# Performance work log

Measured on AMD Instinct MI355X. Metric: run time of the kernel, lower is better.

Reference implementation:

```python
import jax, jax.numpy as jnp
import numpy as np

D_K = 1024
NHEADS = 16
HEAD_DIM = D_K // NHEADS  # 64
STD = float(np.sqrt(HEAD_DIM))  # matches math.sqrt(d_k // nheads)


def setup_inputs() -> dict:
    key = jax.random.key(0)
    ks = jax.random.split(key, 9)
    B, S = 2, 2048
    scale = 1.0 / np.sqrt(D_K)
    x = jax.random.normal(ks[0], (B, S, D_K), dtype=jnp.float32)
    Wq = jax.random.normal(ks[1], (D_K, D_K), dtype=jnp.float32) * scale
    bq = jnp.zeros((D_K,), dtype=jnp.float32)
    Wk = jax.random.normal(ks[2], (D_K, D_K), dtype=jnp.float32) * scale
    bk = jnp.zeros((D_K,), dtype=jnp.float32)
    Wv = jax.random.normal(ks[3], (D_K, D_K), dtype=jnp.float32) * scale
    bv = jnp.zeros((D_K,), dtype=jnp.float32)
    Wo = jax.random.normal(ks[4], (D_K, D_K), dtype=jnp.float32) * scale
    bo = jnp.zeros((D_K,), dtype=jnp.float32)
    return {"x": x, "Wq": Wq, "bq": bq, "Wk": Wk, "bk": bk,
            "Wv": Wv, "bv": bv, "Wo": Wo, "bo": bo}


def _heads(x, W, b):
    # Linear then split heads: (B,S,D) -> (B,H,S,hd)
    B, S, _ = x.shape
    out = x @ W.T + b
    return out.reshape(B, S, NHEADS, HEAD_DIM).transpose(0, 2, 1, 3)


def reference(x, Wq, bq, Wk, bk, Wv, bv, Wo, bo):
    B, S, _ = x.shape
    q = _heads(x, Wq, bq)  # (B,H,S,hd)
    k = _heads(x, Wk, bk)
    v = _heads(x, Wv, bv)
    scores = jnp.einsum('bhqd,bhkd->bhqk', q, k) / STD  # (B,H,S,S)
    causal = jnp.tril(jnp.ones((S, S), dtype=bool))  # mask_factory default
    scores = jnp.where(causal[None, None, :, :], scores, -jnp.inf)
    attn = jax.nn.softmax(scores, axis=-1)
    ctx = jnp.einsum('bhqk,bhkd->bhqd', attn, v)  # (B,H,S,hd)
    ctx = ctx.transpose(0, 2, 1, 3).reshape(B, S, D_K)
    return ctx @ Wo.T + bo
```

## Files before the change

kernel.cpp:

```cpp
#include <hip/hip_runtime.h>
#include <stdint.h>

typedef unsigned short u16;
typedef __bf16 bf16x8 __attribute__((ext_vector_type(8)));
typedef __bf16 bf16x4v __attribute__((ext_vector_type(4)));
typedef float f32x4 __attribute__((ext_vector_type(4)));

typedef __attribute__((address_space(3))) uint32_t lds_u32;
typedef __attribute__((address_space(1))) uint32_t glb_u32;

__device__ __forceinline__ f32x4 mfma16(bf16x8 a, bf16x8 b, f32x4 c) {
    return __builtin_amdgcn_mfma_f32_16x16x32_bf16(a, b, c, 0, 0, 0);
}

__device__ __forceinline__ ushort4 pk4(float a, float b, float c, float d) {
    bf16x4v v;
    v[0] = (__bf16)a; v[1] = (__bf16)b; v[2] = (__bf16)c; v[3] = (__bf16)d;
    union { bf16x4v v; ushort4 u; } cv; cv.v = v; return cv.u;
}

__device__ __forceinline__ float fexp2(float x) {
    return __builtin_amdgcn_exp2f(x);
}

__device__ __forceinline__ void async16(const u16* g, u16* l) {
    __builtin_amdgcn_global_load_lds((glb_u32*)(uintptr_t)(const void*)g,
                                     (lds_u32*)l, 16, 0, 0);
}

__global__ __launch_bounds__(256) void cast_all(
    const float* __restrict__ x,
    const float* __restrict__ w0, const float* __restrict__ w1,
    const float* __restrict__ w2, const float* __restrict__ w3,
    u16* __restrict__ xo, u16* __restrict__ o0, u16* __restrict__ o1,
    u16* __restrict__ o2, u16* __restrict__ o3)
{
    const int s = blockIdx.y;
    const int i = (blockIdx.x * 256 + threadIdx.x) * 4;
    if (s == 0) {
#pragma unroll
        for (int c = 0; c < 4; ++c) {
            const int j = i + c * (1 << 20);
            float4 v = *(const float4*)(x + j);
            *(ushort4*)(xo + j) = pk4(v.x, v.y, v.z, v.w);
        }
    } else {
        const float* in = s == 1 ? w0 : (s == 2 ? w1 : (s == 3 ? w2 : w3));
        u16* out       = s == 1 ? o0 : (s == 2 ? o1 : (s == 3 ? o2 : o3));
        float4 v = *(const float4*)(in + i);
        *(ushort4*)(out + i) = pk4(v.x, v.y, v.z, v.w);
    }
}

__global__ __launch_bounds__(256) void gemm_qkv(
    const u16* __restrict__ A,
    const u16* __restrict__ W0, const u16* __restrict__ W1, const u16* __restrict__ W2,
    const float* __restrict__ B0, const float* __restrict__ B1, const float* __restrict__ B2,
    u16* __restrict__ O0, u16* __restrict__ O1,
    u16* __restrict__ VT,
    int M, int N, int K)
{
    const int x = blockIdx.x & 7;
    const int L = blockIdx.x >> 3;
    const int tm = (8 * (x >> 1) + (L & 7)) << 7;
    const int tnsel = 12 * (x & 1) + (L >> 3);
    const int sel = tnsel >> 3;
    const int tn  = (tnsel & 7) << 7;

    const u16* W      = sel == 0 ? W0 : (sel == 1 ? W1 : W2);
    const float* bias = sel == 0 ? B0 : (sel == 1 ? B1 : B2);
    u16* O            = sel == 0 ? O0 : O1;

    __shared__ __attribute__((aligned(16))) u16 As[128 * 64];
    __shared__ __attribute__((aligned(16))) u16 Bs[128 * 64];
    u16 (*Tb)[136] = (u16 (*)[136])As;

    const int tid  = threadIdx.x;
    const int lane = tid & 63;
    const int w    = tid >> 6;
    const int l15  = lane & 15;
    const int quad = lane >> 4;

    const int wm = (w >> 1) << 6;
    const int wn = (w & 1) << 6;

    f32x4 acc[4][4];
#pragma unroll
    for (int i = 0; i < 4; ++i)
#pragma unroll
        for (int j = 0; j < 4; ++j) acc[i][j] = f32x4{0.f, 0.f, 0.f, 0.f};

    const int lr  = lane >> 3;
    const int lcc = lane & 7;
    const int scc = lcc ^ lr;
    const u16* Ag = A + (size_t)(tm + 32 * w + lr) * K + scc * 8;
    const u16* Wg = W + (size_t)(tn + 32 * w + lr) * K + scc * 8;
    u16* Al = &As[(32 * w + lr) * 64 + lcc * 8];
    u16* Bl = &Bs[(32 * w + lr) * 64 + lcc * 8];

    for (int k0 = 0; k0 < K; k0 += 64) {
        __syncthreads();
#pragma unroll
        for (int m = 0; m < 4; ++m) {
            async16(Ag + k0 + (size_t)m * 8 * K, Al + m * 512);
            async16(Wg + k0 + (size_t)m * 8 * K, Bl + m * 512);
        }
        asm volatile("s_waitcnt vmcnt(0)" ::: "memory");
        __syncthreads();

#pragma unroll
        for (int kk = 0; kk < 2; ++kk) {
            bf16x8 a[4], b[4];
#pragma unroll
            for (int i = 0; i < 4; ++i) {
                const int r  = wm + 16 * i + l15;
                const int sl = (kk * 4 + quad) ^ (r & 7);
                a[i] = *(const bf16x8*)&As[r * 64 + sl * 8];
            }
#pragma unroll
            for (int j = 0; j < 4; ++j) {
                const int r  = wn + 16 * j + l15;
                const int sl = (kk * 4 + quad) ^ (r & 7);
                b[j] = *(const bf16x8*)&Bs[r * 64 + sl * 8];
            }
#pragma unroll
            for (int i = 0; i < 4; ++i)
#pragma unroll
                for (int j = 0; j < 4; ++j)
                    acc[i][j] = mfma16(a[i], b[j], acc[i][j]);
        }
    }

    if (sel == 2) {
        const int bb = tm >> 11;
        const int s0 = tm & 2047;
        const size_t vtb = ((size_t)bb << 10) + tn;
        for (int c32 = 0; c32 < 128; c32 += 32) {
            __syncthreads();
            if ((c32 >> 6) == (wn >> 6)) {
                const int j0 = (c32 >> 4) & 2;
#pragma unroll
                for (int jj = 0; jj < 2; ++jj) {
                    const int j  = j0 + jj;
                    const int cc = jj * 16 + l15;
                    const float bj = bias[tn + wn + 16 * j + l15];
#pragma unroll
                    for (int i = 0; i < 4; ++i) {
                        const int rr = wm + 16 * i + quad * 4;
                        *(ushort4*)&Tb[cc][rr] =
                            pk4(acc[i][j][0] + bj, acc[i][j][1] + bj,
                                acc[i][j][2] + bj, acc[i][j][3] + bj);
                    }
                }
            }
            __syncthreads();
            {
                const int c  = tid >> 3;
                const int ss = (tid & 7) * 16;
                uint4 v0 = *(const uint4*)&Tb[c][ss];
                uint4 v1 = *(const uint4*)&Tb[c][ss + 8];
                u16* dst = &VT[(vtb + c32 + c) * 2048 + s0 + ss];
                *(uint4*)dst       = v0;
                *(uint4*)(dst + 8) = v1;
            }
        }
    } else {
#pragma unroll
        for (int j = 0; j < 4; ++j) {
            const int col = tn + wn + 16 * j + l15;
            const float bj = bias[col];
#pragma unroll
            for (int i = 0; i < 4; ++i) {
                const int row = tm + wm + 16 * i + quad * 4;
#pragma unroll
                for (int r = 0; r < 4; ++r) {
                    union { float f; unsigned u; } v; v.f = acc[i][j][r] + bj;
                    unsigned rn = v.u + 0x7FFFu + ((v.u >> 16) & 1u);
                    O[(size_t)(row + r) * N + col] = (u16)(rn >> 16);
                }
            }
        }
    }
}

__global__ __launch_bounds__(256) void gemm_out64(
    const u16* __restrict__ A, const u16* __restrict__ W,
    const float* __restrict__ bias, float* __restrict__ O,
    int M, int N, int K)
{
    __shared__ __attribute__((aligned(16))) u16 As[128 * 64];
    __shared__ __attribute__((aligned(16))) u16 Bs[64 * 64];

    const int x = blockIdx.x & 7;
    const int L = blockIdx.x >> 3;
    const int tm = (8 * (x >> 1) + (L & 7)) << 7;
    const int tn = (8 * (x & 1) + (L >> 3)) << 6;

    const int tid  = threadIdx.x;
    const int lane = tid & 63;
    const int w    = tid >> 6;
    const int l15  = lane & 15;
    const int quad = lane >> 4;

    const int wm = (w >> 1) << 6;
    const int wn = (w & 1) << 5;

    f32x4 acc[4][2];
#pragma unroll
    for (int i = 0; i < 4; ++i)
#pragma unroll
        for (int j = 0; j < 2; ++j) acc[i][j] = f32x4{0.f, 0.f, 0.f, 0.f};

    const int lr  = lane >> 3;
    const int lcc = lane & 7;
    const int scc = lcc ^ lr;
    const u16* Ag = A + (size_t)(tm + 32 * w + lr) * K + scc * 8;
    const u16* Wg = W + (size_t)(tn + 16 * w + lr) * K + scc * 8;
    u16* Al = &As[(32 * w + lr) * 64 + lcc * 8];
    u16* Bl = &Bs[(16 * w + lr) * 64 + lcc * 8];

    for (int k0 = 0; k0 < K; k0 += 64) {
        __syncthreads();
#pragma unroll
        for (int m = 0; m < 4; ++m)
            async16(Ag + k0 + (size_t)m * 8 * K, Al + m * 512);
#pragma unroll
        for (int m = 0; m < 2; ++m)
            async16(Wg + k0 + (size_t)m * 8 * K, Bl + m * 512);
        asm volatile("s_waitcnt vmcnt(0)" ::: "memory");
        __syncthreads();

#pragma unroll
        for (int kk = 0; kk < 2; ++kk) {
            bf16x8 a[4], b[2];
#pragma unroll
            for (int i = 0; i < 4; ++i) {
                const int r  = wm + 16 * i + l15;
                const int sl = (kk * 4 + quad) ^ (r & 7);
                a[i] = *(const bf16x8*)&As[r * 64 + sl * 8];
            }
#pragma unroll
            for (int j = 0; j < 2; ++j) {
                const int r  = wn + 16 * j + l15;
                const int sl = (kk * 4 + quad) ^ (r & 7);
                b[j] = *(const bf16x8*)&Bs[r * 64 + sl * 8];
            }
#pragma unroll
            for (int i = 0; i < 4; ++i)
#pragma unroll
                for (int j = 0; j < 2; ++j)
                    acc[i][j] = mfma16(a[i], b[j], acc[i][j]);
        }
    }

#pragma unroll
    for (int j = 0; j < 2; ++j) {
        const int col = tn + wn + 16 * j + l15;
        const float bj = bias[col];
#pragma unroll
        for (int i = 0; i < 4; ++i) {
            const int row = tm + wm + 16 * i + quad * 4;
#pragma unroll
            for (int r = 0; r < 4; ++r)
                O[(size_t)(row + r) * N + col] = acc[i][j][r] + bj;
        }
    }
}

__device__ __forceinline__ bf16x8 rdt(const u16* base, int t, int l15, int cc) {
    const int r = t * 16 + l15;
    const int c = (cc & 3) ^ ((r >> 1) & 3);
    return *(const bf16x8*)(base + (cc >> 2) * 2048 + r * 32 + c * 8);
}

#define QK_EXP(Z, PROW, QG, MASKED, RSV, KB)                                   \
    do {                                                                       \
        _Pragma("unroll")                                                      \
        for (int t = 0; t < 4; ++t) {                                          \
            float e0 = fexp2(fmaf((Z)[t][0], SC, -16.0f));                     \
            float e1 = fexp2(fmaf((Z)[t][1], SC, -16.0f));                     \
            float e2 = fexp2(fmaf((Z)[t][2], SC, -16.0f));                     \
            float e3 = fexp2(fmaf((Z)[t][3], SC, -16.0f));                     \
            if (MASKED) {                                                      \
                const int kb = (KB) + t * 16 + quad * 4;                       \
                if (kb + 0 > (QG)) e0 = 0.f;                                   \
                if (kb + 1 > (QG)) e1 = 0.f;                                   \
                if (kb + 2 > (QG)) e2 = 0.f;                                   \
                if (kb + 3 > (QG)) e3 = 0.f;                                   \
            }                                                                  \
            (RSV)[0] += e0; (RSV)[1] += e1;                                    \
            (RSV)[2] += e2; (RSV)[3] += e3;                                    \
            *(ushort4*)((PROW) + (((2 * t + whi) ^ sl7) << 3) + woff) =        \
                pk4(e0, e1, e2, e3);                                           \
        }                                                                      \
    } while (0)

__global__ __launch_bounds__(256) void attn8(
    const u16* __restrict__ Q, const u16* __restrict__ Kb,
    const u16* __restrict__ VT, u16* __restrict__ ctx)
{
    __shared__ __attribute__((aligned(16))) u16 Kt[2][4096];
    __shared__ __attribute__((aligned(16))) u16 Vt[3][4096];
    __shared__ __attribute__((aligned(16))) u16 Pt[4][32][64];

    const int tid  = threadIdx.x;
    const int lane = tid & 63;
    const int wid  = tid >> 6;
    const int l15  = lane & 15;
    const int quad = lane >> 4;
    const int sl7  = l15 & 7;
    const int whi  = quad >> 1;
    const int woff = (quad & 1) * 4;

    const int hb = blockIdx.x & 31;
    const int h  = hb & 15, b = hb >> 4;
    const int ti = blockIdx.x >> 5;
    const int g  = (ti & 1) ? (15 - (ti >> 1)) : (ti >> 1);

    const int sL = 4 * g + wid, sH = 127 - sL;
    const int KL = g, KH = 31 - g;

    const size_t rowbase = (size_t)b * 2048;
    const int cbase = h * 64;
    const u16* kbase = Kb + rowbase * 1024 + cbase;
    const u16* vbase = VT + ((size_t)b * 1024 + cbase) * 2048;

    const int qgL = sL * 16 + l15, qgH = sH * 16 + l15;
    const u16* qpL = Q + (rowbase + qgL) * 1024 + cbase + quad * 8;
    const u16* qpH = Q + (rowbase + qgH) * 1024 + cbase + quad * 8;
    const bf16x8 qL0 = *(const bf16x8*)qpL, qL1 = *(const bf16x8*)(qpL + 32);
    const bf16x8 qH0 = *(const bf16x8*)qpH, qH1 = *(const bf16x8*)(qpH + 32);

    const int sr  = tid >> 2;
    const int sc0 = (((tid & 3) ^ ((sr >> 1) & 3)) << 3);
    const u16* kg = kbase + (size_t)sr * 1024 + sc0;
    const u16* vg = vbase + (size_t)sr * 2048 + sc0;

    f32x4 oL[4], oH[4];
#pragma unroll
    for (int i = 0; i < 4; ++i) { oL[i] = f32x4{0,0,0,0}; oH[i] = f32x4{0,0,0,0}; }
    f32x4 rsLv = {0,0,0,0}, rsHv = {0,0,0,0};
    const float SC = 0.18033688011112042f;

    u16 (*ptw)[64] = Pt[wid];
    u16* const prH = &ptw[16 + l15][0];
    u16* const prL = &ptw[l15][0];

    async16(kg,      &Kt[0][tid * 8]);
    async16(kg + 32, &Kt[0][2048 + tid * 8]);
    async16(vg,      &Vt[0][tid * 8]);
    async16(vg + 32, &Vt[0][2048 + tid * 8]);

    bf16x8 pbH0 = {}, pbH1 = {}, pbL0 = {}, pbL1 = {};
    bool doLp = false;
    int c3 = 0;

    for (int kt = 0; kt <= KH; ++kt) {
        const int curK = kt & 1, nxtK = curK ^ 1;
        const int n3 = (c3 == 2) ? 0 : c3 + 1;
        const int p3 = 3 - c3 - n3;
        asm volatile("s_waitcnt vmcnt(0)" ::: "memory");
        __syncthreads();
        if (kt < KH) {
            const u16* kgn = kg + (size_t)(kt + 1) * 65536;
            const u16* vgn = vg + (kt + 1) * 64;
            async16(kgn,      &Kt[nxtK][tid * 8]);
            async16(kgn + 32, &Kt[nxtK][2048 + tid * 8]);
            async16(vgn,      &Vt[n3][tid * 8]);
            async16(vgn + 32, &Vt[n3][2048 + tid * 8]);
        }
        const u16* KT = Kt[curK];
        const bool doL = (kt <= KL);
        const bool mH = (kt == KH), mL = (kt == KL);

        f32x4 zH[4], zL[4];
        __builtin_amdgcn_s_setprio(1);
        if (doL) {
#pragma unroll
            for (int t = 0; t < 4; ++t) {
                const bf16x8 kA = rdt(KT, t, l15, quad);
                const bf16x8 kB = rdt(KT, t, l15, quad + 4);
                f32x4 zh = {0,0,0,0};
                zh = mfma16(kA, qH0, zh);
                zh = mfma16(kB, qH1, zh);
                zH[t] = zh;
                f32x4 zl = {0,0,0,0};
                zl = mfma16(kA, qL0, zl);
                zl = mfma16(kB, qL1, zl);
                zL[t] = zl;
            }
        } else {
#pragma unroll
            for (int t = 0; t < 4; ++t) {
                const bf16x8 kA = rdt(KT, t, l15, quad);
                const bf16x8 kB = rdt(KT, t, l15, quad + 4);
                f32x4 zh = {0,0,0,0};
                zh = mfma16(kA, qH0, zh);
                zh = mfma16(kB, qH1, zh);
                zH[t] = zh;
            }
        }
        if (kt > 0) {
            const u16* VP = Vt[p3];
            if (doLp) {
#pragma unroll
                for (int t = 0; t < 4; ++t) {
                    const bf16x8 vA = rdt(VP, t, l15, quad);
                    const bf16x8 vB = rdt(VP, t, l15, quad + 4);
                    oH[t] = mfma16(vA, pbH0, oH[t]);
                    oH[t] = mfma16(vB, pbH1, oH[t]);
                    oL[t] = mfma16(vA, pbL0, oL[t]);
                    oL[t] = mfma16(vB, pbL1, oL[t]);
                }
            } else {
#pragma unroll
                for (int t = 0; t < 4; ++t) {
                    const bf16x8 vA = rdt(VP, t, l15, quad);
                    const bf16x8 vB = rdt(VP, t, l15, quad + 4);
                    oH[t] = mfma16(vA, pbH0, oH[t]);
                    oH[t] = mfma16(vB, pbH1, oH[t]);
                }
            }
        }
        __builtin_amdgcn_s_setprio(0);

        const int ktb = kt * 64;
        if (mH) QK_EXP(zH, prH, qgH, 1, rsHv, ktb);
        else    QK_EXP(zH, prH, qgH, 0, rsHv, ktb);
        if (doL) {
            if (mL) QK_EXP(zL, prL, qgL, 1, rsLv, ktb);
            else    QK_EXP(zL, prL, qgL, 0, rsLv, ktb);
        }

        pbH0 = *(const bf16x8*)(prH + ((quad ^ sl7) << 3));
        pbH1 = *(const bf16x8*)(prH + (((quad | 4) ^ sl7) << 3));
        if (doL) {
            pbL0 = *(const bf16x8*)(prL + ((quad ^ sl7) << 3));
            pbL1 = *(const bf16x8*)(prL + (((quad | 4) ^ sl7) << 3));
        }
        doLp = doL;
        c3 = n3;
    }

    {
        const int epi3 = (c3 == 0) ? 2 : c3 - 1;
        const u16* VP = Vt[epi3];
        __builtin_amdgcn_s_setprio(1);
#pragma unroll
        for (int t = 0; t < 4; ++t) {
            const bf16x8 vA = rdt(VP, t, l15, quad);
            const bf16x8 vB = rdt(VP, t, l15, quad + 4);
            oH[t] = mfma16(vA, pbH0, oH[t]);
            oH[t] = mfma16(vB, pbH1, oH[t]);
        }
        __builtin_amdgcn_s_setprio(0);
    }

    float rsH = (rsHv[0] + rsHv[1]) + (rsHv[2] + rsHv[3]);
    float rsL = (rsLv[0] + rsLv[1]) + (rsLv[2] + rsLv[3]);
    rsH += __shfl_xor(rsH, 16); rsH += __shfl_xor(rsH, 32);
    rsL += __shfl_xor(rsL, 16); rsL += __shfl_xor(rsL, 32);
    const float iH = 1.0f / rsH, iL = 1.0f / rsL;
#pragma unroll
    for (int t = 0; t < 4; ++t) {
        *(ushort4*)&ctx[(rowbase + qgL) * 1024 + cbase + t * 16 + quad * 4] =
            pk4(oL[t][0] * iL, oL[t][1] * iL, oL[t][2] * iL, oL[t][3] * iL);
        *(ushort4*)&ctx[(rowbase + qgH) * 1024 + cbase + t * 16 + quad * 4] =
            pk4(oH[t][0] * iH, oH[t][1] * iH, oH[t][2] * iH, oH[t][3] * iH);
    }
}

extern "C" void kernel_launch(void* const* d_in, const int* in_sizes, int n_in,
                              void* d_out, int out_size, void* d_ws, size_t ws_size,
                              hipStream_t stream) {
    const float* x  = (const float*)d_in[0];
    const float* Wq = (const float*)d_in[1];
    const float* bq = (const float*)d_in[2];
    const float* Wk = (const float*)d_in[3];
    const float* bk = (const float*)d_in[4];
    const float* Wv = (const float*)d_in[5];
    const float* bv = (const float*)d_in[6];
    const float* Wo = (const float*)d_in[7];
    const float* bo = (const float*)d_in[8];
    float* out = (float*)d_out;

    const int N = 1024, K = 1024;
    const int M = in_sizes[0] / K;
    const size_t MN = (size_t)M * N;
    const size_t WN = (size_t)N * K;

    u16* xb  = (u16*)d_ws;
    u16* wqb = xb  + MN;
    u16* wkb = wqb + WN;
    u16* wvb = wkb + WN;
    u16* wob = wvb + WN;
    u16* q   = wob + WN;
    u16* kb  = q   + MN;
    u16* vt  = kb  + MN;
    u16* ctx = q;

    cast_all<<<dim3(1024, 5), 256, 0, stream>>>(
        x, Wq, Wk, Wv, Wo, xb, wqb, wkb, wvb, wob);

    gemm_qkv<<<dim3(768), 256, 0, stream>>>(
        xb, wqb, wkb, wvb, bq, bk, bv, q, kb, vt, M, N, K);

    attn8<<<dim3(512), 256, 0, stream>>>(q, kb, vt, ctx);

    gemm_out64<<<dim3(512), 256, 0, stream>>>(
        ctx, wob, bo, out, M, N, K);
}
```

Measured before the change: 192.8 us.

## Double-buffer LDS tiles in QKV and output projection GEMMs

Both projection GEMM kernels now hold two LDS buffers for their A and W tiles. Each iteration waits for the current tile, synchronises, then issues async loads for the next K-tile into the other buffer before running MFMAs on the current one. Global-to-LDS load latency can then overlap with matrix compute, where before each tile was loaded and then waited on. The cost is doubled shared memory per block (64 KB for the QKV kernel), which may reduce the number of resident blocks per CU.

```diff
diff --git a/kernel.cpp b/kernel.cpp
--- a/kernel.cpp
+++ b/kernel.cpp
@@ -71,8 +71,8 @@
     const float* bias = sel == 0 ? B0 : (sel == 1 ? B1 : B2);
     u16* O            = sel == 0 ? O0 : O1;
 
-    __shared__ __attribute__((aligned(16))) u16 As[128 * 64];
-    __shared__ __attribute__((aligned(16))) u16 Bs[128 * 64];
+    __shared__ __attribute__((aligned(16))) u16 As[2][128 * 64];
+    __shared__ __attribute__((aligned(16))) u16 Bs[2][128 * 64];
     u16 (*Tb)[136] = (u16 (*)[136])As;
 
     const int tid  = threadIdx.x;
@@ -95,19 +95,27 @@
     const int scc = lcc ^ lr;
     const u16* Ag = A + (size_t)(tm + 32 * w + lr) * K + scc * 8;
     const u16* Wg = W + (size_t)(tn + 32 * w + lr) * K + scc * 8;
-    u16* Al = &As[(32 * w + lr) * 64 + lcc * 8];
-    u16* Bl = &Bs[(32 * w + lr) * 64 + lcc * 8];
-
-    for (int k0 = 0; k0 < K; k0 += 64) {
-        __syncthreads();
-#pragma unroll
-        for (int m = 0; m < 4; ++m) {
-            async16(Ag + k0 + (size_t)m * 8 * K, Al + m * 512);
-            async16(Wg + k0 + (size_t)m * 8 * K, Bl + m * 512);
-        }
+    u16* Al = &As[0][(32 * w + lr) * 64 + lcc * 8];
+    u16* Bl = &Bs[0][(32 * w + lr) * 64 + lcc * 8];
+
+#define QKV_STAGE(bi, k0)                                                      \
+    do {                                                                       \
+        _Pragma("unroll")                                                      \
+        for (int m = 0; m < 4; ++m) {                                          \
+            async16(Ag + (k0) + (size_t)m * 8 * K, Al + (bi) * 8192 + m * 512);\
+            async16(Wg + (k0) + (size_t)m * 8 * K, Bl + (bi) * 8192 + m * 512);\
+        }                                                                      \
+    } while (0)
+
+    const int nt = K >> 6;
+    QKV_STAGE(0, 0);
+    for (int t = 0; t < nt; ++t) {
+        const int cur = t & 1;
         asm volatile("s_waitcnt vmcnt(0)" ::: "memory");
         __syncthreads();
-
+        if (t + 1 < nt) QKV_STAGE(cur ^ 1, (t + 1) * 64);
+        const u16* Ab = As[cur];
+        const u16* Bb = Bs[cur];
 #pragma unroll
         for (int kk = 0; kk < 2; ++kk) {
             bf16x8 a[4], b[4];
@@ -115,13 +123,13 @@
             for (int i = 0; i < 4; ++i) {
                 const int r  = wm + 16 * i + l15;
                 const int sl = (kk * 4 + quad) ^ (r & 7);
-                a[i] = *(const bf16x8*)&As[r * 64 + sl * 8];
+                a[i] = *(const bf16x8*)&Ab[r * 64 + sl * 8];
             }
 #pragma unroll
             for (int j = 0; j < 4; ++j) {
                 const int r  = wn + 16 * j + l15;
                 const int sl = (kk * 4 + quad) ^ (r & 7);
-                b[j] = *(const bf16x8*)&Bs[r * 64 + sl * 8];
+                b[j] = *(const bf16x8*)&Bb[r * 64 + sl * 8];
             }
 #pragma unroll
             for (int i = 0; i < 4; ++i)
@@ -130,6 +138,7 @@
                     acc[i][j] = mfma16(a[i], b[j], acc[i][j]);
         }
     }
+#undef QKV_STAGE
 
     if (sel == 2) {
         const int bb = tm >> 11;
@@ -188,8 +197,8 @@
     const float* __restrict__ bias, float* __restrict__ O,
     int M, int N, int K)
 {
-    __shared__ __attribute__((aligned(16))) u16 As[128 * 64];
-    __shared__ __attribute__((aligned(16))) u16 Bs[64 * 64];
+    __shared__ __attribute__((aligned(16))) u16 As[2][128 * 64];
+    __shared__ __attribute__((aligned(16))) u16 Bs[2][64 * 64];
 
     const int x = blockIdx.x & 7;
     const int L = blockIdx.x >> 3;
@@ -216,20 +225,28 @@
     const int scc = lcc ^ lr;
     const u16* Ag = A + (size_t)(tm + 32 * w + lr) * K + scc * 8;
     const u16* Wg = W + (size_t)(tn + 16 * w + lr) * K + scc * 8;
-    u16* Al = &As[(32 * w + lr) * 64 + lcc * 8];
-    u16* Bl = &Bs[(16 * w + lr) * 64 + lcc * 8];
-
-    for (int k0 = 0; k0 < K; k0 += 64) {
-        __syncthreads();
-#pragma unroll
-        for (int m = 0; m < 4; ++m)
-            async16(Ag + k0 + (size_t)m * 8 * K, Al + m * 512);
-#pragma unroll
-        for (int m = 0; m < 2; ++m)
-            async16(Wg + k0 + (size_t)m * 8 * K, Bl + m * 512);
+    u16* Al = &As[0][(32 * w + lr) * 64 + lcc * 8];
+    u16* Bl = &Bs[0][(16 * w + lr) * 64 + lcc * 8];
+
+#define OUT_STAGE(bi, k0)                                                      \
+    do {                                                                       \
+        _Pragma("unroll")                                                      \
+        for (int m = 0; m < 4; ++m)                                            \
+            async16(Ag + (k0) + (size_t)m * 8 * K, Al + (bi) * 8192 + m * 512);\
+        _Pragma("unroll")                                                      \
+        for (int m = 0; m < 2; ++m)                                            \
+            async16(Wg + (k0) + (size_t)m * 8 * K, Bl + (bi) * 4096 + m * 512);\
+    } while (0)
+
+    const int nt = K >> 6;
+    OUT_STAGE(0, 0);
+    for (int t = 0; t < nt; ++t) {
+        const int cur = t & 1;
         asm volatile("s_waitcnt vmcnt(0)" ::: "memory");
         __syncthreads();
-
+        if (t + 1 < nt) OUT_STAGE(cur ^ 1, (t + 1) * 64);
+        const u16* Ab = As[cur];
+        const u16* Bb = Bs[cur];
 #pragma unroll
         for (int kk = 0; kk < 2; ++kk) {
             bf16x8 a[4], b[2];
@@ -237,13 +254,13 @@
             for (int i = 0; i < 4; ++i) {
                 const int r  = wm + 16 * i + l15;
                 const int sl = (kk * 4 + quad) ^ (r & 7);
-                a[i] = *(const bf16x8*)&As[r * 64 + sl * 8];
+                a[i] = *(const bf16x8*)&Ab[r * 64 + sl * 8];
             }
 #pragma unroll
             for (int j = 0; j < 2; ++j) {
                 const int r  = wn + 16 * j + l15;
                 const int sl = (kk * 4 + quad) ^ (r & 7);
-                b[j] = *(const bf16x8*)&Bs[r * 64 + sl * 8];
+                b[j] = *(const bf16x8*)&Bb[r * 64 + sl * 8];
             }
 #pragma unroll
             for (int i = 0; i < 4; ++i)
@@ -252,6 +269,7 @@
                     acc[i][j] = mfma16(a[i], b[j], acc[i][j]);
         }
     }
+#undef OUT_STAGE
 
 #pragma unroll
     for (int j = 0; j < 2; ++j) {
```

Measured after the change: 188.4 us. 2.3% less time.
